# Kernel optimization log

Hardware: AMD Instinct MI355X
Metric: run time of the kernel (lower is better)

## Reference

```python
import jax, jax.numpy as jnp
import numpy as np

# Canonical Mamba-1 block dims
D_MODEL = 1024
D_INNER = 2048        # d_model * projection_size (expand=2)
D_STATE = 16          # SSM state size N (Mamba default)
DT_RANK = 64          # d_model // 16 (Mamba default)
KER = 4               # conv_ker
BATCH, SEQ = 2, 1024


def setup_inputs() -> dict:
    key = jax.random.key(0)
    ks = jax.random.split(key, 8)
    sc = lambda k, shape, s: (jax.random.normal(k, shape, dtype=jnp.float32) * s)
    A_log = jnp.log(jnp.broadcast_to(
        jnp.arange(1, D_STATE + 1, dtype=jnp.float32), (D_INNER, D_STATE)))
    return {
        "hidden_states": jax.random.normal(ks[0], (BATCH, SEQ, D_MODEL), dtype=jnp.float32),
        "in_proj_w": sc(ks[1], (D_MODEL, 2 * D_INNER), 0.02),
        "conv_w": sc(ks[2], (D_INNER, 1, KER), 0.1),      # depthwise conv kernel [O, I/groups=1, K]
        "conv_b": jnp.zeros((D_INNER,), dtype=jnp.float32),
        "x_proj_w": sc(ks[3], (D_INNER, DT_RANK + 2 * D_STATE), 0.02),
        "dt_proj_w": sc(ks[4], (DT_RANK, D_INNER), 0.05),
        "dt_proj_b": jnp.full((D_INNER,), -4.6, dtype=jnp.float32),  # softplus(-4.6) ~ 0.01 init dt
        "A_log": A_log,
        "D_skip": jnp.ones((D_INNER,), dtype=jnp.float32),
        "out_proj_w": sc(ks[5], (D_INNER, D_MODEL), 0.02),
    }


def _selective_scan(u, delta, A, Bm, Cm, D_skip):
    """u, delta: [B,L,D]; A: [D,N]; Bm, Cm: [B,L,N]; D_skip: [D]."""
    # Discretize: seq-major for lax.scan
    dA = jnp.exp(jnp.einsum('bld,dn->lbdn', delta, A))            # [L,B,D,N]
    dBu = jnp.einsum('bld,bln,bld->lbdn', delta, Bm, u)           # [L,B,D,N]

    def step(h, ab):
        dA_t, dBu_t = ab
        h = dA_t * h + dBu_t
        return h, h

    h0 = jnp.zeros((u.shape[0], A.shape[0], A.shape[1]), u.dtype)  # [B,D,N]
    _, hs = jax.lax.scan(step, h0, (dA, dBu))                      # hs: [L,B,D,N]
    y = jnp.einsum('lbdn,bln->bld', hs, Cm)
    return y + u * D_skip


def reference(hidden_states, in_proj_w, conv_w, conv_b, x_proj_w,
              dt_proj_w, dt_proj_b, A_log, D_skip, out_proj_w):
    silu = jax.nn.silu
    # Input projection -> (x, res), each [B,L,D_INNER]
    xz = hidden_states @ in_proj_w
    x, res = jnp.split(xz, 2, axis=-1)

    # Causal depthwise conv over sequence: [B,D,L] layout
    x_c = jnp.transpose(x, (0, 2, 1))
    x_c = jax.lax.conv_general_dilated(
        x_c, conv_w, window_strides=(1,), padding=[(KER - 1, 0)],
        dimension_numbers=('NCH', 'OIH', 'NCH'), feature_group_count=D_INNER)
    x_c = x_c + conv_b[None, :, None]
    x = silu(jnp.transpose(x_c, (0, 2, 1)))                        # [B,L,D_INNER]

    # SSM parameterization
    x_dbl = x @ x_proj_w                                           # [B,L,dt_rank+2N]
    dt, Bm, Cm = jnp.split(x_dbl, [DT_RANK, DT_RANK + D_STATE], axis=-1)
    delta = jax.nn.softplus(dt @ dt_proj_w + dt_proj_b)            # [B,L,D_INNER]
    A = -jnp.exp(A_log)                                            # [D_INNER, N]

    y = _selective_scan(x, delta, A, Bm, Cm, D_skip)

    # SiLU gate and output projection
    y = y * silu(res)
    return y @ out_proj_w
```

## Files before the change

kernel.cpp:

```cpp
#include <hip/hip_runtime.h>
#include <hip/hip_bf16.h>
#include <cstdint>

#define D_MODEL  1024
#define D_INNER  2048
#define D_STATE  16
#define DT_RANK  64
#define KERW     4
#define BATCH    2
#define SEQ      1024
#define NTOK     (BATCH * SEQ)
#define CHUNKS   32
#define LOG2C    5
#define LC       (SEQ / CHUNKS)

typedef _Float16 h8 __attribute__((ext_vector_type(8)));
typedef _Float16 h4 __attribute__((ext_vector_type(4)));
typedef float    f32x4 __attribute__((ext_vector_type(4)));

__device__ __forceinline__ float siluf(float x) {
    return x / (1.f + __expf(-x));
}

#define GLOAD_LDS16(g, p) __builtin_amdgcn_global_load_lds( \
    (const __attribute__((address_space(1))) void*)(g),      \
    (__attribute__((address_space(3))) void*)(p), 16, 0, 0)

__global__ __launch_bounds__(256)
void f32_to_f16_k(const float* __restrict__ in, _Float16* __restrict__ out, int n4)
{
    int i = blockIdx.x * 256 + threadIdx.x;
    if (i >= n4) return;
    float4 v = ((const float4*)in)[i];
    h4 h = { (_Float16)v.x, (_Float16)v.y, (_Float16)v.z, (_Float16)v.w };
    *(h4*)(out + (size_t)i * 4) = h;
}

template<int NN>
__global__ __launch_bounds__(256)
void pack_b_f16(const float* __restrict__ B, _Float16* __restrict__ Bp, int K)
{
    constexpr int SH = (NN == 4096) ? 12 : 10;
    int gid = blockIdx.x * 256 + threadIdx.x;
    int n  = gid & (NN - 1);
    int kb = gid >> SH;
    h8 v;
    #pragma unroll
    for (int j = 0; j < 8; ++j)
        v[j] = (_Float16)B[(size_t)(kb * 8 + j) * NN + n];
    *(h8*)(Bp + (size_t)gid * 8) = v;
}

__device__ __forceinline__ void stage_tiles(
    const _Float16* __restrict__ A, const _Float16* __restrict__ Bp,
    _Float16* as, _Float16* bs, int bm, int bn, int k0, int N, int lda, int tid)
{
    #pragma unroll
    for (int i = 0; i < 2; ++i) {
        int c = i * 256 + tid;
        int row = c & 127, kgc = c >> 7;
        const _Float16* g = A + (size_t)(bm + row) * lda + k0 + kgc * 8;
        GLOAD_LDS16(g, as + (size_t)c * 8);
    }
    {
        int c = tid;
        int col = c & 63, kgc = c >> 6;
        const _Float16* g = Bp + ((size_t)((k0 >> 3) + kgc) * N + bn + col) * 8;
        GLOAD_LDS16(g, bs + (size_t)c * 8);
    }
}

__global__ __launch_bounds__(256)
void gemm_f16_mfma(const _Float16* __restrict__ A, const _Float16* __restrict__ Bp,
                   float* __restrict__ C, int M, int N, int K, int lda, int ldc)
{
    __shared__ alignas(16) _Float16 As[2][4 * 128 * 8];
    __shared__ alignas(16) _Float16 Bs[2][4 * 64 * 8];

    const int tid = threadIdx.x;
    const int l = tid & 63, w = tid >> 6;
    const int wm = w >> 1, wn = w & 1;

    const int nwg = gridDim.x;
    const int qch = nwg >> 3;
    const int wg  = ((blockIdx.x & 7) * qch) + (blockIdx.x >> 3);
    const int nbn = N >> 6;
    const int bn  = (wg % nbn) * 64;
    const int bm  = (wg / nbn) * 128;

    const int kslice = K / gridDim.z;
    const int kbeg = blockIdx.z * kslice;
    const int kend = kbeg + kslice;

    f32x4 acc[4][2] = {};
    const int kg = l >> 4, r = l & 15;

    stage_tiles(A, Bp, As[0], Bs[0], bm, bn, kbeg, N, lda, tid);
    __syncthreads();

    int cur = 0;
    for (int k0 = kbeg; k0 < kend; k0 += 32) {
        if (k0 + 32 < kend)
            stage_tiles(A, Bp, As[cur ^ 1], Bs[cur ^ 1], bm, bn, k0 + 32, N, lda, tid);

        h8 a[4], b[2];
        #pragma unroll
        for (int mi = 0; mi < 4; ++mi)
            a[mi] = *(const h8*)(As[cur] + (size_t)(kg * 128 + wm * 64 + mi * 16 + r) * 8);
        #pragma unroll
        for (int ni = 0; ni < 2; ++ni)
            b[ni] = *(const h8*)(Bs[cur] + (size_t)(kg * 64 + wn * 32 + ni * 16 + r) * 8);

        #pragma unroll
        for (int mi = 0; mi < 4; ++mi)
            #pragma unroll
            for (int ni = 0; ni < 2; ++ni)
                acc[mi][ni] = __builtin_amdgcn_mfma_f32_16x16x32_f16(
                    a[mi], b[ni], acc[mi][ni], 0, 0, 0);

        __syncthreads();
        cur ^= 1;
    }

    float* dst = C + (size_t)blockIdx.z * M * ldc;
    const int q = l >> 4;
    #pragma unroll
    for (int mi = 0; mi < 4; ++mi)
        #pragma unroll
        for (int ni = 0; ni < 2; ++ni)
            #pragma unroll
            for (int j = 0; j < 4; ++j)
                dst[(size_t)(bm + wm * 64 + mi * 16 + q * 4 + j) * ldc
                    + (bn + wn * 32 + ni * 16 + r)] = acc[mi][ni][j];
}

template<bool BIAS, bool SOFTPLUS>
__global__ __launch_bounds__(256)
void gemm_f32(const float* __restrict__ A, const float* __restrict__ B,
              const float* __restrict__ bias, float* __restrict__ C,
              int M, int N, int K, int lda, int ldb, int ldc)
{
    __shared__ float As[16][68];
    __shared__ float Bs[16][68];
    const int tid = threadIdx.x;
    const int tx = tid & 15, ty = tid >> 4;
    const int bm = blockIdx.y * 64, bn = blockIdx.x * 64;

    float acc[4][4] = {};

    const int ar  = tid >> 2;
    const int ac4 = (tid & 3) << 2;
    const int bkr = tid >> 4;
    const int bc4 = (tid & 15) << 2;

    for (int k0 = 0; k0 < K; k0 += 16) {
        float4 av = make_float4(0.f, 0.f, 0.f, 0.f);
        {
            int row = bm + ar;
            if (row < M)
                av = *(const float4*)(A + (size_t)row * lda + (k0 + ac4));
        }
        As[ac4 + 0][ar] = av.x; As[ac4 + 1][ar] = av.y;
        As[ac4 + 2][ar] = av.z; As[ac4 + 3][ar] = av.w;

        float4 bv = make_float4(0.f, 0.f, 0.f, 0.f);
        {
            int col = bn + bc4;
            const float* bp = B + (size_t)(k0 + bkr) * ldb + col;
            if (col + 3 < N) {
                bv = *(const float4*)bp;
            } else {
                if (col + 0 < N) bv.x = bp[0];
                if (col + 1 < N) bv.y = bp[1];
                if (col + 2 < N) bv.z = bp[2];
                if (col + 3 < N) bv.w = bp[3];
            }
        }
        Bs[bkr][bc4 + 0] = bv.x; Bs[bkr][bc4 + 1] = bv.y;
        Bs[bkr][bc4 + 2] = bv.z; Bs[bkr][bc4 + 3] = bv.w;

        __syncthreads();

        #pragma unroll
        for (int kk = 0; kk < 16; ++kk) {
            float a[4], b[4];
            #pragma unroll
            for (int i = 0; i < 4; ++i) a[i] = As[kk][ty * 4 + i];
            #pragma unroll
            for (int j = 0; j < 4; ++j) b[j] = Bs[kk][tx * 4 + j];
            #pragma unroll
            for (int i = 0; i < 4; ++i)
                #pragma unroll
                for (int j = 0; j < 4; ++j)
                    acc[i][j] = fmaf(a[i], b[j], acc[i][j]);
        }
        __syncthreads();
    }

    #pragma unroll
    for (int i = 0; i < 4; ++i) {
        int row = bm + ty * 4 + i;
        if (row >= M) continue;
        #pragma unroll
        for (int j = 0; j < 4; ++j) {
            int col = bn + tx * 4 + j;
            if (col >= N) continue;
            float v = acc[i][j];
            if (BIAS) v += bias[col];
            if (SOFTPLUS) v = (v > 20.f) ? v : log1pf(__expf(v));
            C[(size_t)row * ldc + col] = v;
        }
    }
}

__global__ __launch_bounds__(256)
void gemm_f32_splitk(const float* __restrict__ A, const float* __restrict__ B,
                     float* __restrict__ part,
                     int M, int N, int K, int lda, int ldb, int ldc)
{
    __shared__ float As[16][68];
    __shared__ float Bs[16][68];
    const int tid = threadIdx.x;
    const int tx = tid & 15, ty = tid >> 4;
    const int bm = blockIdx.y * 64, bn = blockIdx.x * 64;
    const int kslice = K / gridDim.z;
    const int kbeg = blockIdx.z * kslice;

    float acc[4][4] = {};

    const int ar  = tid >> 2;
    const int ac4 = (tid & 3) << 2;
    const int bkr = tid >> 4;
    const int bc4 = (tid & 15) << 2;

    for (int k0 = kbeg; k0 < kbeg + kslice; k0 += 16) {
        float4 av;
        {
            int row = bm + ar;
            av = *(const float4*)(A + (size_t)row * lda + (k0 + ac4));
        }
        As[ac4 + 0][ar] = av.x; As[ac4 + 1][ar] = av.y;
        As[ac4 + 2][ar] = av.z; As[ac4 + 3][ar] = av.w;

        float4 bv = make_float4(0.f, 0.f, 0.f, 0.f);
        {
            int col = bn + bc4;
            const float* bp = B + (size_t)(k0 + bkr) * ldb + col;
            if (col + 3 < N) {
                bv = *(const float4*)bp;
            } else {
                if (col + 0 < N) bv.x = bp[0];
                if (col + 1 < N) bv.y = bp[1];
                if (col + 2 < N) bv.z = bp[2];
                if (col + 3 < N) bv.w = bp[3];
            }
        }
        Bs[bkr][bc4 + 0] = bv.x; Bs[bkr][bc4 + 1] = bv.y;
        Bs[bkr][bc4 + 2] = bv.z; Bs[bkr][bc4 + 3] = bv.w;

        __syncthreads();

        #pragma unroll
        for (int kk = 0; kk < 16; ++kk) {
            float a[4], b[4];
            #pragma unroll
            for (int i = 0; i < 4; ++i) a[i] = As[kk][ty * 4 + i];
            #pragma unroll
            for (int j = 0; j < 4; ++j) b[j] = Bs[kk][tx * 4 + j];
            #pragma unroll
            for (int i = 0; i < 4; ++i)
                #pragma unroll
                for (int j = 0; j < 4; ++j)
                    acc[i][j] = fmaf(a[i], b[j], acc[i][j]);
        }
        __syncthreads();
    }

    float* dst = part + (size_t)blockIdx.z * M * ldc;
    #pragma unroll
    for (int i = 0; i < 4; ++i) {
        int row = bm + ty * 4 + i;
        #pragma unroll
        for (int j = 0; j < 4; ++j) {
            int col = bn + tx * 4 + j;
            if (col >= N) continue;
            dst[(size_t)row * ldc + col] = acc[i][j];
        }
    }
}

__global__ __launch_bounds__(256)
void reduce_splitk(const float* __restrict__ part, float* __restrict__ out,
                   int n, int S)
{
    int i = blockIdx.x * 256 + threadIdx.x;
    if (i >= n) return;
    float s = 0.f;
    for (int j = 0; j < S; ++j) s += part[(size_t)j * n + i];
    out[i] = s;
}

__global__ __launch_bounds__(256)
void conv_silu(const float* __restrict__ xz, const float* __restrict__ conv_w,
               const float* __restrict__ conv_b, float* __restrict__ u)
{
    int idx = blockIdx.x * 256 + threadIdx.x;
    if (idx >= NTOK * D_INNER) return;
    int d = idx & (D_INNER - 1);
    int t = idx >> 11;
    int l = t & (SEQ - 1);
    int b = t >> 10;

    float w0 = conv_w[d * 4 + 0], w1 = conv_w[d * 4 + 1];
    float w2 = conv_w[d * 4 + 2], w3 = conv_w[d * 4 + 3];

    const float* base = xz + (size_t)b * SEQ * (2 * D_INNER) + d;
    float acc = conv_b[d];
    if (l >= 3) acc += w0 * base[(size_t)(l - 3) * (2 * D_INNER)];
    if (l >= 2) acc += w1 * base[(size_t)(l - 2) * (2 * D_INNER)];
    if (l >= 1) acc += w2 * base[(size_t)(l - 1) * (2 * D_INNER)];
    acc += w3 * base[(size_t)l * (2 * D_INNER)];

    u[idx] = siluf(acc);
}

__global__ __launch_bounds__(256)
void scan_pass1(const float* __restrict__ delta, const float* __restrict__ u,
                const float* __restrict__ xdbl, const float* __restrict__ A_log,
                float* __restrict__ Aprod, float* __restrict__ Hend)
{
    int gid = blockIdx.x * 256 + threadIdx.x;
    if (gid >= BATCH * CHUNKS * D_INNER * 2) return;
    int lane = gid & 63;
    int wv   = gid >> 6;
    int dsub = lane & 31, nh = lane >> 5;
    int dblk = wv & 63;
    int c    = (wv >> 6) & (CHUNKS - 1);
    int b    = wv >> (6 + LOG2C);
    int d    = dblk * 32 + dsub;

    float An[8];
    {
        const float4* a4 = (const float4*)(A_log + d * 16 + nh * 8);
        #pragma unroll
        for (int q = 0; q < 2; ++q) {
            float4 v = a4[q];
            An[q * 4 + 0] = -__expf(v.x);
            An[q * 4 + 1] = -__expf(v.y);
            An[q * 4 + 2] = -__expf(v.z);
            An[q * 4 + 3] = -__expf(v.w);
        }
    }

    const float* dp = delta + ((size_t)b * SEQ + c * LC) * D_INNER + d;
    const float* up = u     + ((size_t)b * SEQ + c * LC) * D_INNER + d;
    const float* xb = xdbl  + ((size_t)b * SEQ + c * LC) * 96 + DT_RANK + nh * 8;

    float h[8], ap[8];
    #pragma unroll
    for (int n = 0; n < 8; ++n) { h[n] = 0.f; ap[n] = 1.f; }

    float  dt = dp[0], ut = up[0];
    float4 Bq0 = *(const float4*)(xb);
    float4 Bq1 = *(const float4*)(xb + 4);

    for (int l = 0; l < LC - 1; ++l) {
        float  dt_n = dp[(size_t)(l + 1) * D_INNER];
        float  ut_n = up[(size_t)(l + 1) * D_INNER];
        float4 B0n  = *(const float4*)(xb + (l + 1) * 96);
        float4 B1n  = *(const float4*)(xb + (l + 1) * 96 + 4);

        float Bv[8] = { Bq0.x, Bq0.y, Bq0.z, Bq0.w, Bq1.x, Bq1.y, Bq1.z, Bq1.w };
        float dtu = dt * ut;
        #pragma unroll
        for (int n = 0; n < 8; ++n) {
            float da = __expf(dt * An[n]);
            h[n]  = fmaf(da, h[n], dtu * Bv[n]);
            ap[n] *= da;
        }
        dt = dt_n; ut = ut_n; Bq0 = B0n; Bq1 = B1n;
    }
    {
        float Bv[8] = { Bq0.x, Bq0.y, Bq0.z, Bq0.w, Bq1.x, Bq1.y, Bq1.z, Bq1.w };
        float dtu = dt * ut;
        #pragma unroll
        for (int n = 0; n < 8; ++n) {
            float da = __expf(dt * An[n]);
            h[n]  = fmaf(da, h[n], dtu * Bv[n]);
            ap[n] *= da;
        }
    }

    size_t off = ((((size_t)b * CHUNKS + c) * D_INNER) + d) * 16 + nh * 8;
    *(float4*)(Hend  + off)     = make_float4(h[0], h[1], h[2], h[3]);
    *(float4*)(Hend  + off + 4) = make_float4(h[4], h[5], h[6], h[7]);
    *(float4*)(Aprod + off)     = make_float4(ap[0], ap[1], ap[2], ap[3]);
    *(float4*)(Aprod + off + 4) = make_float4(ap[4], ap[5], ap[6], ap[7]);
}

__global__ __launch_bounds__(256)
void scan_pass2(const float* __restrict__ Aprod, float* __restrict__ HendHin)
{
    int idx = blockIdx.x * 256 + threadIdx.x;
    if (idx >= BATCH * D_INNER * D_STATE) return;
    int n = idx & 15;
    int d = (idx >> 4) & (D_INNER - 1);
    int b = idx >> 15;

    float h = 0.f;
    for (int c = 0; c < CHUNKS; ++c) {
        size_t j = ((((size_t)b * CHUNKS + c) * D_INNER) + d) * 16 + n;
        float ap = Aprod[j];
        float he = HendHin[j];
        HendHin[j] = h;
        h = ap * h + he;
    }
}

__global__ __launch_bounds__(256)
void scan_pass3(const float* __restrict__ delta, const float* __restrict__ u,
                const float* __restrict__ xdbl, const float* __restrict__ xz,
                const float* __restrict__ A_log, const float* __restrict__ D_skip,
                const float* __restrict__ Hin, _Float16* __restrict__ ygh)
{
    int gid = blockIdx.x * 256 + threadIdx.x;
    if (gid >= BATCH * CHUNKS * D_INNER * 2) return;
    int lane = gid & 63;
    int wv   = gid >> 6;
    int dsub = lane & 31, nh = lane >> 5;
    int dblk = wv & 63;
    int c    = (wv >> 6) & (CHUNKS - 1);
    int b    = wv >> (6 + LOG2C);
    int d    = dblk * 32 + dsub;

    float An[8];
    {
        const float4* a4 = (const float4*)(A_log + d * 16 + nh * 8);
        #pragma unroll
        for (int q = 0; q < 2; ++q) {
            float4 v = a4[q];
            An[q * 4 + 0] = -__expf(v.x);
            An[q * 4 + 1] = -__expf(v.y);
            An[q * 4 + 2] = -__expf(v.z);
            An[q * 4 + 3] = -__expf(v.w);
        }
    }
    float Dd = D_skip[d];

    float h[8];
    {
        size_t off = ((((size_t)b * CHUNKS + c) * D_INNER) + d) * 16 + nh * 8;
        float4 v0 = *(const float4*)(Hin + off);
        float4 v1 = *(const float4*)(Hin + off + 4);
        h[0] = v0.x; h[1] = v0.y; h[2] = v0.z; h[3] = v0.w;
        h[4] = v1.x; h[5] = v1.y; h[6] = v1.z; h[7] = v1.w;
    }

    const float* dp = delta + ((size_t)b * SEQ + c * LC) * D_INNER + d;
    const float* up = u     + ((size_t)b * SEQ + c * LC) * D_INNER + d;
    const float* xb = xdbl  + ((size_t)b * SEQ + c * LC) * 96 + DT_RANK + nh * 8;
    const float* rp = xz    + ((size_t)b * SEQ + c * LC) * (2 * D_INNER) + D_INNER + d;
    _Float16*    yp = ygh   + ((size_t)b * SEQ + c * LC) * 8192 + d;

    float  dt = dp[0], ut = up[0], res = rp[0];
    float4 Bq0 = *(const float4*)(xb);
    float4 Bq1 = *(const float4*)(xb + 4);
    float4 Cq0 = *(const float4*)(xb + 16);
    float4 Cq1 = *(const float4*)(xb + 20);

    for (int l = 0; l < LC; ++l) {
        float dt_n, ut_n, res_n;
        float4 B0n, B1n, C0n, C1n;
        if (l + 1 < LC) {
            dt_n  = dp[(size_t)(l + 1) * D_INNER];
            ut_n  = up[(size_t)(l + 1) * D_INNER];
            res_n = rp[(size_t)(l + 1) * (2 * D_INNER)];
            B0n = *(const float4*)(xb + (l + 1) * 96);
            B1n = *(const float4*)(xb + (l + 1) * 96 + 4);
            C0n = *(const float4*)(xb + (l + 1) * 96 + 16);
            C1n = *(const float4*)(xb + (l + 1) * 96 + 20);
        }

        float Bv[8] = { Bq0.x, Bq0.y, Bq0.z, Bq0.w, Bq1.x, Bq1.y, Bq1.z, Bq1.w };
        float Cv[8] = { Cq0.x, Cq0.y, Cq0.z, Cq0.w, Cq1.x, Cq1.y, Cq1.z, Cq1.w };
        float dtu = dt * ut;
        float y = 0.f;
        #pragma unroll
        for (int n = 0; n < 8; ++n) {
            float da = __expf(dt * An[n]);
            h[n] = fmaf(da, h[n], dtu * Bv[n]);
            y = fmaf(h[n], Cv[n], y);
        }
        y += __shfl_xor(y, 32, 64);
        if (nh == 0)
            yp[(size_t)l * 8192] = (_Float16)((y + ut * Dd) * siluf(res));

        dt = dt_n; ut = ut_n; res = res_n;
        Bq0 = B0n; Bq1 = B1n; Cq0 = C0n; Cq1 = C1n;
    }
}

extern "C" void kernel_launch(void* const* d_in, const int* in_sizes, int n_in,
                              void* d_out, int out_size, void* d_ws, size_t ws_size,
                              hipStream_t stream)
{
    const float* H      = (const float*)d_in[0];
    const float* Win    = (const float*)d_in[1];
    const float* convw  = (const float*)d_in[2];
    const float* convb  = (const float*)d_in[3];
    const float* xprojw = (const float*)d_in[4];
    const float* dtw    = (const float*)d_in[5];
    const float* dtb    = (const float*)d_in[6];
    const float* Alog   = (const float*)d_in[7];
    const float* Dskip  = (const float*)d_in[8];
    const float* Wout   = (const float*)d_in[9];
    float* out = (float*)d_out;

    float* ws    = (float*)d_ws;
    float* xz    = ws;
    float* u     = xz   + (size_t)NTOK * 4096;
    float* xdbl  = u    + (size_t)NTOK * 2048;
    float* delta = xdbl + (size_t)NTOK * 96;
    float* Aprod = delta + (size_t)NTOK * 2048;
    float* Hend  = Aprod + (size_t)BATCH * CHUNKS * D_INNER * 16;

    _Float16* Hh    = (_Float16*)delta;
    _Float16* Winp  = (_Float16*)delta + 2 * 1024 * 1024;
    float*    part  = delta;
    float*    part4 = delta;
    _Float16* ygh   = (_Float16*)xz;
    _Float16* Woutp = (_Float16*)Aprod;

    dim3 blk(256);

    f32_to_f16_k<<<(NTOK * D_MODEL / 4) / 256, blk, 0, stream>>>(H, Hh, NTOK * D_MODEL / 4);
    pack_b_f16<4096><<<((D_MODEL / 8) * 4096) / 256, blk, 0, stream>>>(Win, Winp, D_MODEL);

    gemm_f16_mfma<<<dim3((4096 / 64) * (NTOK / 128), 1, 1), blk, 0, stream>>>(
        Hh, Winp, xz, NTOK, 2 * D_INNER, D_MODEL, D_MODEL, 2 * D_INNER);

    conv_silu<<<(NTOK * D_INNER) / 256, blk, 0, stream>>>(xz, convw, convb, u);

    gemm_f32_splitk<<<dim3(2, NTOK / 64, 16), blk, 0, stream>>>(
        u, xprojw, part, NTOK, 96, D_INNER, D_INNER, 96, 96);
    reduce_splitk<<<(NTOK * 96 + 255) / 256, blk, 0, stream>>>(
        part, xdbl, NTOK * 96, 16);

    gemm_f32<true, true><<<dim3(D_INNER / 64, NTOK / 64), blk, 0, stream>>>(
        xdbl, dtw, dtb, delta, NTOK, D_INNER, DT_RANK, 96, D_INNER, D_INNER);

    {
        int nthr2 = BATCH * CHUNKS * D_INNER * 2;
        scan_pass1<<<nthr2 / 256, blk, 0, stream>>>(delta, u, xdbl, Alog, Aprod, Hend);
        scan_pass2<<<(BATCH * D_INNER * 16) / 256, blk, 0, stream>>>(Aprod, Hend);
        scan_pass3<<<nthr2 / 256, blk, 0, stream>>>(delta, u, xdbl, xz, Alog, Dskip,
                                                    Hend , ygh);
    }

    pack_b_f16<1024><<<((D_INNER / 8) * 1024) / 256, blk, 0, stream>>>(Wout, Woutp, D_INNER);

    gemm_f16_mfma<<<dim3((1024 / 64) * (NTOK / 128), 1, 2), blk, 0, stream>>>(
        ygh, Woutp, part4, NTOK, D_MODEL, D_INNER, 8192, D_MODEL);
    reduce_splitk<<<(NTOK * D_MODEL) / 256, blk, 0, stream>>>(
        part4, out, NTOK * D_MODEL, 2);
}
```

Baseline: 290.8 us.

## Fuse conv+SiLU into x_proj GEMM and scan passes, merge prep kernels

Removes the standalone conv_silu kernel and the u buffer. The causal depthwise conv and SiLU are now recomputed on the fly inside the x_proj split-K GEMM A-tile load and inside both scan passes, using a sliding window of four xz values. The three fp16 conversion/pack kernels are merged into one launch, and ygh gets a dense stride in a separate workspace slot. This cuts an 8M-element write and re-read plus two launches, at the cost of redundant conv work (four strided loads per A element in the GEMM) and extra per-step ALU in the scans.

```diff
diff --git a/kernel.cpp b/kernel.cpp
--- a/kernel.cpp
+++ b/kernel.cpp
@@ -27,28 +27,36 @@
     (__attribute__((address_space(3))) void*)(p), 16, 0, 0)
 
 __global__ __launch_bounds__(256)
-void f32_to_f16_k(const float* __restrict__ in, _Float16* __restrict__ out, int n4)
-{
-    int i = blockIdx.x * 256 + threadIdx.x;
-    if (i >= n4) return;
-    float4 v = ((const float4*)in)[i];
-    h4 h = { (_Float16)v.x, (_Float16)v.y, (_Float16)v.z, (_Float16)v.w };
-    *(h4*)(out + (size_t)i * 4) = h;
-}
-
-template<int NN>
-__global__ __launch_bounds__(256)
-void pack_b_f16(const float* __restrict__ B, _Float16* __restrict__ Bp, int K)
-{
-    constexpr int SH = (NN == 4096) ? 12 : 10;
-    int gid = blockIdx.x * 256 + threadIdx.x;
-    int n  = gid & (NN - 1);
-    int kb = gid >> SH;
-    h8 v;
-    #pragma unroll
-    for (int j = 0; j < 8; ++j)
-        v[j] = (_Float16)B[(size_t)(kb * 8 + j) * NN + n];
-    *(h8*)(Bp + (size_t)gid * 8) = v;
+void prep_kernel(const float* __restrict__ H, const float* __restrict__ Win,
+                 const float* __restrict__ Wout, _Float16* __restrict__ Hh,
+                 _Float16* __restrict__ Winp, _Float16* __restrict__ Woutp)
+{
+    int bid = blockIdx.x;
+    int tid = threadIdx.x;
+    if (bid < 2048) {
+        int i = bid * 256 + tid;
+        float4 v = ((const float4*)H)[i];
+        h4 h = { (_Float16)v.x, (_Float16)v.y, (_Float16)v.z, (_Float16)v.w };
+        *(h4*)(Hh + (size_t)i * 4) = h;
+    } else if (bid < 4096) {
+        int gid = (bid - 2048) * 256 + tid;
+        int n  = gid & 4095;
+        int kb = gid >> 12;
+        h8 v;
+        #pragma unroll
+        for (int j = 0; j < 8; ++j)
+            v[j] = (_Float16)Win[(size_t)(kb * 8 + j) * 4096 + n];
+        *(h8*)(Winp + (size_t)gid * 8) = v;
+    } else {
+        int gid = (bid - 4096) * 256 + tid;
+        int n  = gid & 1023;
+        int kb = gid >> 10;
+        h8 v;
+        #pragma unroll
+        for (int j = 0; j < 8; ++j)
+            v[j] = (_Float16)Wout[(size_t)(kb * 8 + j) * 1024 + n];
+        *(h8*)(Woutp + (size_t)gid * 8) = v;
+    }
 }
 
 __device__ __forceinline__ void stage_tiles(
@@ -214,16 +222,16 @@
 }
 
 __global__ __launch_bounds__(256)
-void gemm_f32_splitk(const float* __restrict__ A, const float* __restrict__ B,
-                     float* __restrict__ part,
-                     int M, int N, int K, int lda, int ldb, int ldc)
+void gemm2_conv_splitk(const float* __restrict__ xz, const float* __restrict__ convw,
+                       const float* __restrict__ convb, const float* __restrict__ B,
+                       float* __restrict__ part)
 {
     __shared__ float As[16][68];
     __shared__ float Bs[16][68];
     const int tid = threadIdx.x;
     const int tx = tid & 15, ty = tid >> 4;
     const int bm = blockIdx.y * 64, bn = blockIdx.x * 64;
-    const int kslice = K / gridDim.z;
+    const int kslice = D_INNER / gridDim.z;
     const int kbeg = blockIdx.z * kslice;
 
     float acc[4][4] = {};
@@ -234,29 +242,44 @@
     const int bc4 = (tid & 15) << 2;
 
     for (int k0 = kbeg; k0 < kbeg + kslice; k0 += 16) {
-        float4 av;
         {
             int row = bm + ar;
-            av = *(const float4*)(A + (size_t)row * lda + (k0 + ac4));
-        }
-        As[ac4 + 0][ar] = av.x; As[ac4 + 1][ar] = av.y;
-        As[ac4 + 2][ar] = av.z; As[ac4 + 3][ar] = av.w;
-
-        float4 bv = make_float4(0.f, 0.f, 0.f, 0.f);
+            int d0  = k0 + ac4;
+            int lpos = row & (SEQ - 1);
+            const float* xr = xz + (size_t)row * 4096 + d0;
+            float4 x0  = *(const float4*)xr;
+            float4 xm1 = make_float4(0.f, 0.f, 0.f, 0.f), xm2 = xm1, xm3 = xm1;
+            if (lpos >= 1) xm1 = *(const float4*)(xr - 4096);
+            if (lpos >= 2) xm2 = *(const float4*)(xr - 8192);
+            if (lpos >= 3) xm3 = *(const float4*)(xr - 12288);
+            float4 cb = *(const float4*)(convb + d0);
+            float4 c0 = *(const float4*)(convw + (size_t)(d0 + 0) * 4);
+            float4 c1 = *(const float4*)(convw + (size_t)(d0 + 1) * 4);
+            float4 c2 = *(const float4*)(convw + (size_t)(d0 + 2) * 4);
+            float4 c3 = *(const float4*)(convw + (size_t)(d0 + 3) * 4);
+            float4 av;
+            av.x = siluf(cb.x + c0.x * xm3.x + c0.y * xm2.x + c0.z * xm1.x + c0.w * x0.x);
+            av.y = siluf(cb.y + c1.x * xm3.y + c1.y * xm2.y + c1.z * xm1.y + c1.w * x0.y);
+            av.z = siluf(cb.z + c2.x * xm3.z + c2.y * xm2.z + c2.z * xm1.z + c2.w * x0.z);
+            av.w = siluf(cb.w + c3.x * xm3.w + c3.y * xm2.w + c3.z * xm1.w + c3.w * x0.w);
+            As[ac4 + 0][ar] = av.x; As[ac4 + 1][ar] = av.y;
+            As[ac4 + 2][ar] = av.z; As[ac4 + 3][ar] = av.w;
+        }
         {
             int col = bn + bc4;
-            const float* bp = B + (size_t)(k0 + bkr) * ldb + col;
-            if (col + 3 < N) {
+            float4 bv = make_float4(0.f, 0.f, 0.f, 0.f);
+            const float* bp = B + (size_t)(k0 + bkr) * 96 + col;
+            if (col + 3 < 96) {
                 bv = *(const float4*)bp;
             } else {
-                if (col + 0 < N) bv.x = bp[0];
-                if (col + 1 < N) bv.y = bp[1];
-                if (col + 2 < N) bv.z = bp[2];
-                if (col + 3 < N) bv.w = bp[3];
+                if (col + 0 < 96) bv.x = bp[0];
+                if (col + 1 < 96) bv.y = bp[1];
+                if (col + 2 < 96) bv.z = bp[2];
+                if (col + 3 < 96) bv.w = bp[3];
             }
-        }
-        Bs[bkr][bc4 + 0] = bv.x; Bs[bkr][bc4 + 1] = bv.y;
-        Bs[bkr][bc4 + 2] = bv.z; Bs[bkr][bc4 + 3] = bv.w;
+            Bs[bkr][bc4 + 0] = bv.x; Bs[bkr][bc4 + 1] = bv.y;
+            Bs[bkr][bc4 + 2] = bv.z; Bs[bkr][bc4 + 3] = bv.w;
+        }
 
         __syncthreads();
 
@@ -276,15 +299,15 @@
         __syncthreads();
     }
 
-    float* dst = part + (size_t)blockIdx.z * M * ldc;
+    float* dst = part + (size_t)blockIdx.z * NTOK * 96;
     #pragma unroll
     for (int i = 0; i < 4; ++i) {
         int row = bm + ty * 4 + i;
         #pragma unroll
         for (int j = 0; j < 4; ++j) {
             int col = bn + tx * 4 + j;
-            if (col >= N) continue;
-            dst[(size_t)row * ldc + col] = acc[i][j];
+            if (col >= 96) continue;
+            dst[(size_t)row * 96 + col] = acc[i][j];
         }
     }
 }
@@ -301,31 +324,8 @@
 }
 
 __global__ __launch_bounds__(256)
-void conv_silu(const float* __restrict__ xz, const float* __restrict__ conv_w,
-               const float* __restrict__ conv_b, float* __restrict__ u)
-{
-    int idx = blockIdx.x * 256 + threadIdx.x;
-    if (idx >= NTOK * D_INNER) return;
-    int d = idx & (D_INNER - 1);
-    int t = idx >> 11;
-    int l = t & (SEQ - 1);
-    int b = t >> 10;
-
-    float w0 = conv_w[d * 4 + 0], w1 = conv_w[d * 4 + 1];
-    float w2 = conv_w[d * 4 + 2], w3 = conv_w[d * 4 + 3];
-
-    const float* base = xz + (size_t)b * SEQ * (2 * D_INNER) + d;
-    float acc = conv_b[d];
-    if (l >= 3) acc += w0 * base[(size_t)(l - 3) * (2 * D_INNER)];
-    if (l >= 2) acc += w1 * base[(size_t)(l - 2) * (2 * D_INNER)];
-    if (l >= 1) acc += w2 * base[(size_t)(l - 1) * (2 * D_INNER)];
-    acc += w3 * base[(size_t)l * (2 * D_INNER)];
-
-    u[idx] = siluf(acc);
-}
-
-__global__ __launch_bounds__(256)
-void scan_pass1(const float* __restrict__ delta, const float* __restrict__ u,
+void scan_pass1(const float* __restrict__ delta, const float* __restrict__ xz,
+                const float* __restrict__ convw, const float* __restrict__ convb,
                 const float* __restrict__ xdbl, const float* __restrict__ A_log,
                 float* __restrict__ Aprod, float* __restrict__ Hend)
 {
@@ -351,25 +351,36 @@
             An[q * 4 + 3] = -__expf(v.w);
         }
     }
+    float4 cw = *(const float4*)(convw + (size_t)d * 4);
+    float  cb = convb[d];
 
     const float* dp = delta + ((size_t)b * SEQ + c * LC) * D_INNER + d;
-    const float* up = u     + ((size_t)b * SEQ + c * LC) * D_INNER + d;
+    const float* xp = xz    + ((size_t)b * SEQ + c * LC) * 4096 + d;
     const float* xb = xdbl  + ((size_t)b * SEQ + c * LC) * 96 + DT_RANK + nh * 8;
 
     float h[8], ap[8];
     #pragma unroll
     for (int n = 0; n < 8; ++n) { h[n] = 0.f; ap[n] = 1.f; }
 
-    float  dt = dp[0], ut = up[0];
+    float xw1 = 0.f, xw2 = 0.f, xw3 = 0.f;
+    if (c > 0) {
+        xw1 = xp[-4096];
+        xw2 = xp[-2 * 4096];
+        xw3 = xp[-3 * 4096];
+    }
+
+    float  dt = dp[0];
+    float  x0 = xp[0];
     float4 Bq0 = *(const float4*)(xb);
     float4 Bq1 = *(const float4*)(xb + 4);
 
     for (int l = 0; l < LC - 1; ++l) {
         float  dt_n = dp[(size_t)(l + 1) * D_INNER];
-        float  ut_n = up[(size_t)(l + 1) * D_INNER];
+        float  x0n  = xp[(size_t)(l + 1) * 4096];
         float4 B0n  = *(const float4*)(xb + (l + 1) * 96);
         float4 B1n  = *(const float4*)(xb + (l + 1) * 96 + 4);
 
+        float ut = siluf(cb + cw.x * xw3 + cw.y * xw2 + cw.z * xw1 + cw.w * x0);
         float Bv[8] = { Bq0.x, Bq0.y, Bq0.z, Bq0.w, Bq1.x, Bq1.y, Bq1.z, Bq1.w };
         float dtu = dt * ut;
         #pragma unroll
@@ -378,9 +389,11 @@
             h[n]  = fmaf(da, h[n], dtu * Bv[n]);
             ap[n] *= da;
         }
-        dt = dt_n; ut = ut_n; Bq0 = B0n; Bq1 = B1n;
+        xw3 = xw2; xw2 = xw1; xw1 = x0; x0 = x0n;
+        dt = dt_n; Bq0 = B0n; Bq1 = B1n;
     }
     {
+        float ut = siluf(cb + cw.x * xw3 + cw.y * xw2 + cw.z * xw1 + cw.w * x0);
         float Bv[8] = { Bq0.x, Bq0.y, Bq0.z, Bq0.w, Bq1.x, Bq1.y, Bq1.z, Bq1.w };
         float dtu = dt * ut;
         #pragma unroll
@@ -418,10 +431,11 @@
 }
 
 __global__ __launch_bounds__(256)
-void scan_pass3(const float* __restrict__ delta, const float* __restrict__ u,
-                const float* __restrict__ xdbl, const float* __restrict__ xz,
-                const float* __restrict__ A_log, const float* __restrict__ D_skip,
-                const float* __restrict__ Hin, _Float16* __restrict__ ygh)
+void scan_pass3(const float* __restrict__ delta, const float* __restrict__ xz,
+                const float* __restrict__ convw, const float* __restrict__ convb,
+                const float* __restrict__ xdbl, const float* __restrict__ A_log,
+                const float* __restrict__ D_skip, const float* __restrict__ Hin,
+                _Float16* __restrict__ ygh)
 {
     int gid = blockIdx.x * 256 + threadIdx.x;
     if (gid >= BATCH * CHUNKS * D_INNER * 2) return;
@@ -445,7 +459,9 @@
             An[q * 4 + 3] = -__expf(v.w);
         }
     }
-    float Dd = D_skip[d];
+    float4 cw = *(const float4*)(convw + (size_t)d * 4);
+    float  cb = convb[d];
+    float  Dd = D_skip[d];
 
     float h[8];
     {
@@ -457,30 +473,38 @@
     }
 
     const float* dp = delta + ((size_t)b * SEQ + c * LC) * D_INNER + d;
-    const float* up = u     + ((size_t)b * SEQ + c * LC) * D_INNER + d;
+    const float* xp = xz    + ((size_t)b * SEQ + c * LC) * 4096 + d;
+    const float* rp = xp + D_INNER;
     const float* xb = xdbl  + ((size_t)b * SEQ + c * LC) * 96 + DT_RANK + nh * 8;
-    const float* rp = xz    + ((size_t)b * SEQ + c * LC) * (2 * D_INNER) + D_INNER + d;
-    _Float16*    yp = ygh   + ((size_t)b * SEQ + c * LC) * 8192 + d;
-
-    float  dt = dp[0], ut = up[0], res = rp[0];
+    _Float16*    yp = ygh   + ((size_t)b * SEQ + c * LC) * 2048 + d;
+
+    float xw1 = 0.f, xw2 = 0.f, xw3 = 0.f;
+    if (c > 0) {
+        xw1 = xp[-4096];
+        xw2 = xp[-2 * 4096];
+        xw3 = xp[-3 * 4096];
+    }
+
+    float  dt = dp[0], x0 = xp[0], res = rp[0];
     float4 Bq0 = *(const float4*)(xb);
     float4 Bq1 = *(const float4*)(xb + 4);
     float4 Cq0 = *(const float4*)(xb + 16);
     float4 Cq1 = *(const float4*)(xb + 20);
 
     for (int l = 0; l < LC; ++l) {
-        float dt_n, ut_n, res_n;
+        float dt_n, x0n, res_n;
         float4 B0n, B1n, C0n, C1n;
         if (l + 1 < LC) {
             dt_n  = dp[(size_t)(l + 1) * D_INNER];
-            ut_n  = up[(size_t)(l + 1) * D_INNER];
-            res_n = rp[(size_t)(l + 1) * (2 * D_INNER)];
+            x0n   = xp[(size_t)(l + 1) * 4096];
+            res_n = rp[(size_t)(l + 1) * 4096];
             B0n = *(const float4*)(xb + (l + 1) * 96);
             B1n = *(const float4*)(xb + (l + 1) * 96 + 4);
             C0n = *(const float4*)(xb + (l + 1) * 96 + 16);
             C1n = *(const float4*)(xb + (l + 1) * 96 + 20);
         }
 
+        float ut = siluf(cb + cw.x * xw3 + cw.y * xw2 + cw.z * xw1 + cw.w * x0);
         float Bv[8] = { Bq0.x, Bq0.y, Bq0.z, Bq0.w, Bq1.x, Bq1.y, Bq1.z, Bq1.w };
         float Cv[8] = { Cq0.x, Cq0.y, Cq0.z, Cq0.w, Cq1.x, Cq1.y, Cq1.z, Cq1.w };
         float dtu = dt * ut;
@@ -493,9 +517,10 @@
         }
         y += __shfl_xor(y, 32, 64);
         if (nh == 0)
-            yp[(size_t)l * 8192] = (_Float16)((y + ut * Dd) * siluf(res));
-
-        dt = dt_n; ut = ut_n; res = res_n;
+            yp[(size_t)l * 2048] = (_Float16)((y + ut * Dd) * siluf(res));
+
+        xw3 = xw2; xw2 = xw1; xw1 = x0; x0 = x0n;
+        dt = dt_n; res = res_n;
         Bq0 = B0n; Bq1 = B1n; Cq0 = C0n; Cq1 = C1n;
     }
 }
@@ -518,8 +543,8 @@
 
     float* ws    = (float*)d_ws;
     float* xz    = ws;
-    float* u     = xz   + (size_t)NTOK * 4096;
-    float* xdbl  = u    + (size_t)NTOK * 2048;
+    float* slotB = xz   + (size_t)NTOK * 4096;
+    float* xdbl  = slotB + (size_t)NTOK * 2048;
     float* delta = xdbl + (size_t)NTOK * 96;
     float* Aprod = delta + (size_t)NTOK * 2048;
     float* Hend  = Aprod + (size_t)BATCH * CHUNKS * D_INNER * 16;
@@ -528,21 +553,18 @@
     _Float16* Winp  = (_Float16*)delta + 2 * 1024 * 1024;
     float*    part  = delta;
     float*    part4 = delta;
-    _Float16* ygh   = (_Float16*)xz;
-    _Float16* Woutp = (_Float16*)Aprod;
+    _Float16* Woutp = (_Float16*)slotB;
+    _Float16* ygh   = (_Float16*)slotB + 2 * 1024 * 1024;
 
     dim3 blk(256);
 
-    f32_to_f16_k<<<(NTOK * D_MODEL / 4) / 256, blk, 0, stream>>>(H, Hh, NTOK * D_MODEL / 4);
-    pack_b_f16<4096><<<((D_MODEL / 8) * 4096) / 256, blk, 0, stream>>>(Win, Winp, D_MODEL);
+    prep_kernel<<<5120, blk, 0, stream>>>(H, Win, Wout, Hh, Winp, Woutp);
 
     gemm_f16_mfma<<<dim3((4096 / 64) * (NTOK / 128), 1, 1), blk, 0, stream>>>(
         Hh, Winp, xz, NTOK, 2 * D_INNER, D_MODEL, D_MODEL, 2 * D_INNER);
 
-    conv_silu<<<(NTOK * D_INNER) / 256, blk, 0, stream>>>(xz, convw, convb, u);
-
-    gemm_f32_splitk<<<dim3(2, NTOK / 64, 16), blk, 0, stream>>>(
-        u, xprojw, part, NTOK, 96, D_INNER, D_INNER, 96, 96);
+    gemm2_conv_splitk<<<dim3(2, NTOK / 64, 16), blk, 0, stream>>>(
+        xz, convw, convb, xprojw, part);
     reduce_splitk<<<(NTOK * 96 + 255) / 256, blk, 0, stream>>>(
         part, xdbl, NTOK * 96, 16);
 
@@ -551,16 +573,16 @@
 
     {
         int nthr2 = BATCH * CHUNKS * D_INNER * 2;
-        scan_pass1<<<nthr2 / 256, blk, 0, stream>>>(delta, u, xdbl, Alog, Aprod, Hend);
+        scan_pass1<<<nthr2 / 256, blk, 0, stream>>>(delta, xz, convw, convb,
+                                                    xdbl, Alog, Aprod, Hend);
         scan_pass2<<<(BATCH * D_INNER * 16) / 256, blk, 0, stream>>>(Aprod, Hend);
-        scan_pass3<<<nthr2 / 256, blk, 0, stream>>>(delta, u, xdbl, xz, Alog, Dskip,
+        scan_pass3<<<nthr2 / 256, blk, 0, stream>>>(delta, xz, convw, convb,
+                                                    xdbl, Alog, Dskip,
                                                     Hend , ygh);
     }
 
-    pack_b_f16<1024><<<((D_INNER / 8) * 1024) / 256, blk, 0, stream>>>(Wout, Woutp, D_INNER);
-
     gemm_f16_mfma<<<dim3((1024 / 64) * (NTOK / 128), 1, 2), blk, 0, stream>>>(
-        ygh, Woutp, part4, NTOK, D_MODEL, D_INNER, 8192, D_MODEL);
+        ygh, Woutp, part4, NTOK, D_MODEL, D_INNER, D_INNER, D_MODEL);
     reduce_splitk<<<(NTOK * D_MODEL) / 256, blk, 0, stream>>>(
         part4, out, NTOK * D_MODEL, 2);
 }
```

Result: no change. 290.4 us (-0.1%).
